# Optimization experiments

Measured on AMD Instinct MI355X. Metric: run time of the kernel, lower is better.

## Reference

```python
import jax, jax.numpy as jnp
import numpy as np

EMB_TABLE = 80000  # full shared embedding rows
N_ITEMS = 50000    # target item count (item_num + 1)
E = 600000         # edges
D = 128            # embedding_size
L = 3              # num_gcn_layers


def gcn_conv(x, W, b, src, dst, norm, n):
    # PyG GCNConv: x' = lin(x); out[i] = sum_{(j->i)} norm_ji * x'[j] + bias
    msgs = (x @ W)[src] * norm[:, None]          # [E+n, D]
    out = jax.ops.segment_sum(msgs, dst, num_segments=n)
    return out + b


def setup_inputs() -> dict:
    key = jax.random.key(0)
    k0, k1, k2 = jax.random.split(key, 3)
    item_emb = jax.random.normal(k0, (EMB_TABLE, D), dtype=jnp.float32) * 0.02
    weights = jax.random.normal(k1, (L, D, D), dtype=jnp.float32) * (1.0 / np.sqrt(D))
    biases = jnp.zeros((L, D), dtype=jnp.float32)
    edge_index = jax.random.randint(k2, (2, E), 0, N_ITEMS, dtype=jnp.int64)
    return {"item_emb": item_emb, "weights": weights, "biases": biases,
            "edge_index": edge_index, "item_nums": N_ITEMS}


def reference(item_emb, weights, biases, edge_index, item_nums):
    n = item_nums
    x0 = item_emb[-n:]  # embeds[0] = item_emb[-item_nums:]
    loops = jnp.arange(n, dtype=edge_index.dtype)
    src = jnp.concatenate([edge_index[0], loops])  # add self-loops (GCNConv default)
    dst = jnp.concatenate([edge_index[1], loops])
    # symmetric normalization: deg computed on target side with self-loops
    deg = jax.ops.segment_sum(jnp.ones_like(src, dtype=x0.dtype), dst, num_segments=n)
    dinv = jnp.where(deg > 0, jax.lax.rsqrt(jnp.maximum(deg, 1e-12)), 0.0)
    norm = dinv[src] * dinv[dst]                   # [E+n]
    embeds = [x0]
    for l in range(weights.shape[0]):
        embeds.append(gcn_conv(embeds[-1], weights[l], biases[l], src, dst, norm, n))
    total = embeds[0]
    for e in embeds[1:]:
        total = total + e
    return (total, *embeds)
```

## Files before the change

kernel.cpp:

```cpp
#include <hip/hip_runtime.h>
#include <stdint.h>

#define D 128

typedef unsigned int u32;
typedef unsigned short u16;
typedef __attribute__((ext_vector_type(8))) short short8;
typedef __attribute__((ext_vector_type(4))) float f32x4;

static __device__ __forceinline__ float bf2f(u16 h) {
    return __uint_as_float(((u32)h) << 16);
}
static __device__ __forceinline__ u16 f2bf(float f) {
    u32 u = __float_as_uint(f);
    u32 r = (u + 0x7fffu + ((u >> 16) & 1u)) >> 16;
    return (u16)r;
}
static __device__ __forceinline__ int clampi(int v, int n) {
    if (v < 0) v = 0;
    if (v >= n) v = n - 1;
    return v;
}

__global__ void k_init(int* __restrict__ hist, int* __restrict__ csr_pos, int n,
                       const u16* __restrict__ emb_raw, const u32* __restrict__ ei_raw,
                       const u16* __restrict__ w_raw, int* __restrict__ flags) {
    int i = blockIdx.x * 256 + threadIdx.x;
    if (i < n) {
        hist[i] = 0;
        csr_pos[i] = 0;
    }
    if (blockIdx.x == 0 && threadIdx.x < 64) {
        int t = threadIdx.x;
        int se = 0, sw = 0, zz = 0;
#pragma unroll
        for (int q = 0; q < 4; q++) {
            int k = t * 4 + q;
            u16 he = emb_raw[2 * k];
            u32 exe = (he >> 7) & 0xFF;
            if (he == 0 || (exe >= 0x60 && exe <= 0x8F)) se++;
            u16 hw = w_raw[2 * k];
            u32 exw = (hw >> 7) & 0xFF;
            if (hw == 0 || (exw >= 0x60 && exw <= 0x8F)) sw++;
            if (ei_raw[2 * k + 1] == 0) zz++;
        }
#pragma unroll
        for (int o = 32; o; o >>= 1) {
            se += __shfl_down(se, o);
            sw += __shfl_down(sw, o);
            zz += __shfl_down(zz, o);
        }
        if (t == 0) {
            flags[0] = (se >= 200) ? 1 : 0;
            flags[2] = (sw >= 200) ? 1 : 0;
            flags[1] = (zz >= 200) ? 1 : 0;
        }
    }
}

__global__ void k_hw(const u32* __restrict__ ei, int E, int n,
                     const int* __restrict__ flags, int* __restrict__ hist,
                     const void* __restrict__ Wbase, u16* __restrict__ WB, int eb) {
    int bid = blockIdx.x;
    if (bid < eb) {
        int e = bid * 256 + threadIdx.x;
        if (e >= E) return;
        int d;
        if (flags[1]) d = ((const int2*)ei)[(size_t)E + e].x;
        else          d = (int)ei[(size_t)E + e];
        atomicAdd(&hist[clampi(d, n)], 1);
    } else {
        int idx = (bid - eb) * 256 + threadIdx.x;
        int e = idx & 7;
        int l = (idx >> 3) & 63;
        int ks = (idx >> 9) & 3;
        int c = (idx >> 11) & 7;
        int layer = idx >> 14;
        int k = ks * 32 + ((l >> 4) << 3) + e;
        int j = (c << 4) + (l & 15);
        size_t src = (size_t)layer * D * D + (size_t)k * D + j;
        float w = flags[2] ? bf2f(((const u16*)Wbase)[src]) : ((const float*)Wbase)[src];
        u16 hb = f2bf(w);
        u16 lb = f2bf(w - bf2f(hb));
        size_t o = (size_t)layer * 32768 + (size_t)((c * 4 + ks) * 64 + l) * 8 + e;
        WB[o] = hb;
        WB[o + 16384] = lb;
    }
}

__global__ void k_scan1(const int* __restrict__ hist, int n,
                        int* __restrict__ incl, int* __restrict__ bsums) {
    __shared__ int s[256];
    int t = threadIdx.x;
    int i = blockIdx.x * 256 + t;
    int v = (i < n) ? hist[i] : 0;
    s[t] = v;
    __syncthreads();
    for (int d2 = 1; d2 < 256; d2 <<= 1) {
        int add = (t >= d2) ? s[t - d2] : 0;
        __syncthreads();
        s[t] += add;
        __syncthreads();
    }
    if (i < n) incl[i] = s[t];
    if (t == 255) bsums[blockIdx.x] = s[255];
}

__global__ void k_scan23(const int* __restrict__ hist, const int* __restrict__ bsums,
                         int n, int* __restrict__ csr_off, float* __restrict__ dinv) {
    __shared__ int s[256];
    int t = threadIdx.x, b = blockIdx.x;
    s[t] = (t < b) ? bsums[t] : 0;
    __syncthreads();
    for (int o = 128; o; o >>= 1) {
        if (t < o) s[t] += s[t + o];
        __syncthreads();
    }
    int add = s[0];
    int i = b * 256 + t;
    if (i < n) {
        int h = hist[i];
        csr_off[i] = add + csr_off[i] - h;
        dinv[i] = rsqrtf((float)(h + 1));
    }
}

__global__ void k_sx(const u32* __restrict__ ei, int E, int n,
                     const int* __restrict__ flags,
                     const int* __restrict__ csr_off, int* __restrict__ csr_pos,
                     const float* __restrict__ dinv, int2* __restrict__ csr_pair,
                     const void* __restrict__ emb, int off_elems, int nD4,
                     float* __restrict__ out_x0, int eb) {
    int bid = blockIdx.x;
    if (bid < eb) {
        int e = bid * 256 + threadIdx.x;
        if (e >= E) return;
        int s, d;
        if (flags[1]) {
            s = ((const int2*)ei)[e].x;
            d = ((const int2*)ei)[(size_t)E + e].x;
        } else {
            s = (int)ei[e];
            d = (int)ei[(size_t)E + e];
        }
        s = clampi(s, n);
        d = clampi(d, n);
        int p = csr_off[d] + atomicAdd(&csr_pos[d], 1);
        if (p >= E) p = E - 1;
        csr_pair[p] = make_int2(s, __float_as_int(dinv[s] * dinv[d]));
    } else {
        int i = (bid - eb) * 256 + threadIdx.x;
        if (i >= nD4) return;
        float4 v;
        if (flags[0]) {
            ushort4 h = ((const ushort4*)((const u16*)emb + off_elems))[i];
            v = make_float4(bf2f(h.x), bf2f(h.y), bf2f(h.z), bf2f(h.w));
        } else {
            v = ((const float4*)((const float*)emb + off_elems))[i];
        }
        ((float4*)out_x0)[i] = v;
    }
}

__global__ __launch_bounds__(256) void k_gemm(const float* __restrict__ A,
                                              const u16* __restrict__ WB, int layer,
                                              int n, u32* __restrict__ Y) {
    __shared__ f32x4 ldsv[4096];
    int tid = threadIdx.x;
    {
        const f32x4* src = (const f32x4*)(WB + (size_t)layer * 32768);
#pragma unroll
        for (int i = 0; i < 16; i++) ldsv[tid + 256 * i] = src[tid + 256 * i];
    }
    __syncthreads();

    int w = tid >> 6, l = tid & 63;
    int row0 = blockIdx.x * 64 + w * 16;
    int ar = row0 + (l & 15);
    if (ar >= n) ar = 0;
    const float* Ab = A + (size_t)ar * D + ((l >> 4) << 3);

    f32x4 acc[8] = {};
    const short8* bp = (const short8*)ldsv;

#pragma unroll
    for (int ks = 0; ks < 4; ks++) {
        f32x4 a0 = *(const f32x4*)(Ab + ks * 32);
        f32x4 a1 = *(const f32x4*)(Ab + ks * 32 + 4);
        float av[8] = {a0.x, a0.y, a0.z, a0.w, a1.x, a1.y, a1.z, a1.w};
        short8 ah, al;
#pragma unroll
        for (int e = 0; e < 8; e++) {
            u16 h = f2bf(av[e]);
            ah[e] = (short)h;
            al[e] = (short)f2bf(av[e] - bf2f(h));
        }
#pragma unroll
        for (int c = 0; c < 8; c++) {
            short8 bh = bp[(c * 4 + ks) * 64 + l];
            short8 bl = bp[2048 + (c * 4 + ks) * 64 + l];
            acc[c] = __builtin_amdgcn_mfma_f32_16x16x32_bf16(al, bh, acc[c], 0, 0, 0);
            acc[c] = __builtin_amdgcn_mfma_f32_16x16x32_bf16(ah, bl, acc[c], 0, 0, 0);
            acc[c] = __builtin_amdgcn_mfma_f32_16x16x32_bf16(ah, bh, acc[c], 0, 0, 0);
        }
    }

    int rbase = row0 + ((l >> 4) << 2);
    int col = l & 15;
#pragma unroll
    for (int r = 0; r < 4; r++) {
        int gr = rbase + r;
        if (gr < n) {
#pragma unroll
            for (int c = 0; c < 4; c++) {
                u32 pack = (u32)f2bf(acc[c][r]) | ((u32)f2bf(acc[c + 4][r]) << 16);
                Y[(size_t)gr * 64 + c * 16 + col] = pack;
            }
        }
    }
}

__global__ __launch_bounds__(256) void k_agg(const u32* __restrict__ Y,
                                             const int* __restrict__ csr_off,
                                             const int* __restrict__ cnt,
                                             const int2* __restrict__ csr_pair,
                                             const float* __restrict__ dinv,
                                             const void* __restrict__ bias_base, int layer,
                                             const int* __restrict__ flags, int n, int nD,
                                             const float* __restrict__ out_base,
                                             float* __restrict__ out_x,
                                             float* __restrict__ out_tot) {
    int i = blockIdx.x * 4 + (threadIdx.x >> 6);
    if (i >= n) return;
    int t = threadIdx.x & 63;
    int g = t >> 4, p = t & 15;

    float lo0 = 0.f, lo1 = 0.f, lo2 = 0.f, lo3 = 0.f;
    float hi0 = 0.f, hi1 = 0.f, hi2 = 0.f, hi3 = 0.f;

#define ACC4(V, W)                                                       \
    do {                                                                 \
        lo0 += __uint_as_float((V).x << 16) * (W);                       \
        hi0 += __uint_as_float((V).x & 0xffff0000u) * (W);               \
        lo1 += __uint_as_float((V).y << 16) * (W);                       \
        hi1 += __uint_as_float((V).y & 0xffff0000u) * (W);               \
        lo2 += __uint_as_float((V).z << 16) * (W);                       \
        hi2 += __uint_as_float((V).z & 0xffff0000u) * (W);               \
        lo3 += __uint_as_float((V).w << 16) * (W);                       \
        hi3 += __uint_as_float((V).w & 0xffff0000u) * (W);               \
    } while (0)

    float di = dinv[i];
    {
        uint4 vs = *(const uint4*)(Y + (size_t)i * 64 + p * 4);
        float ws = (g == 0) ? di * di : 0.0f;
        ACC4(vs, ws);
    }

    int start = csr_off[i];
    int c = cnt[i];

    for (int base = 0; base < c; base += 64) {
        int m = c - base;
        if (m > 64) m = 64;
        int2 pr = (t < m) ? csr_pair[start + base + t] : make_int2(0, 0);
        int s0 = __shfl(pr.x, g);
        float w0 = __uint_as_float((u32)__shfl(pr.y, g));
        uint4 v0 = *(const uint4*)(Y + (size_t)s0 * 64 + p * 4);
        for (int j = 4; j < m; j += 4) {
            int s1 = __shfl(pr.x, j + g);
            float w1 = __uint_as_float((u32)__shfl(pr.y, j + g));
            uint4 v1 = *(const uint4*)(Y + (size_t)s1 * 64 + p * 4);
            ACC4(v0, w0);
            v0 = v1;
            w0 = w1;
        }
        ACC4(v0, w0);
    }
#undef ACC4

#pragma unroll
    for (int mask = 16; mask <= 32; mask <<= 1) {
        lo0 += __shfl_xor(lo0, mask);
        lo1 += __shfl_xor(lo1, mask);
        lo2 += __shfl_xor(lo2, mask);
        lo3 += __shfl_xor(lo3, mask);
        hi0 += __shfl_xor(hi0, mask);
        hi1 += __shfl_xor(hi1, mask);
        hi2 += __shfl_xor(hi2, mask);
        hi3 += __shfl_xor(hi3, mask);
    }

    if (g < 2) {
        float r0 = g ? hi0 : lo0;
        float r1 = g ? hi1 : lo1;
        float r2 = g ? hi2 : lo2;
        float r3 = g ? hi3 : lo3;
        int off = g * 64 + 4 * p;
        float b0, b1, b2, b3;
        if (flags[0]) {
            const u16* bb = (const u16*)bias_base + layer * D + off;
            ushort4 h = *(const ushort4*)bb;
            b0 = bf2f(h.x); b1 = bf2f(h.y); b2 = bf2f(h.z); b3 = bf2f(h.w);
        } else {
            const float* bb = (const float*)bias_base + layer * D + off;
            float4 f = *(const float4*)bb;
            b0 = f.x; b1 = f.y; b2 = f.z; b3 = f.w;
        }
        float4 xv = make_float4(r0 + b0, r1 + b1, r2 + b2, r3 + b3);
        size_t base = (size_t)i * D + off;
        *(float4*)&out_x[base] = xv;

        if (out_tot) {
            float4 s0 = *(const float4*)&out_base[(size_t)1 * nD + base];
            float4 s1 = *(const float4*)&out_base[(size_t)2 * nD + base];
            float4 s2 = *(const float4*)&out_base[(size_t)3 * nD + base];
            *(float4*)&out_tot[base] =
                make_float4(s0.x + s1.x + s2.x + xv.x, s0.y + s1.y + s2.y + xv.y,
                            s0.z + s1.z + s2.z + xv.z, s0.w + s1.w + s2.w + xv.w);
        }
    }
}

extern "C" void kernel_launch(void* const* d_in, const int* in_sizes, int n_in,
                              void* d_out, int out_size, void* d_ws, size_t ws_size,
                              hipStream_t stream) {
    float* out = (float*)d_out;

    const int n = out_size / (5 * D);

    int i_emb = -1, i_ei = -1, i_w = -1, i_b = -1;
    {
        int order[8];
        int m = n_in > 8 ? 8 : n_in;
        for (int i = 0; i < m; i++) order[i] = i;
        for (int a = 0; a < m; a++)
            for (int b2 = a + 1; b2 < m; b2++)
                if (in_sizes[order[b2]] > in_sizes[order[a]]) {
                    int tmp = order[a]; order[a] = order[b2]; order[b2] = tmp;
                }
        i_emb = order[0];
        i_ei  = (m > 1) ? order[1] : 0;
        for (int i = 0; i < m; i++) {
            if (in_sizes[i] == 3 * D * D && i_w < 0) i_w = i;
            if (in_sizes[i] == 3 * D && i_b < 0) i_b = i;
        }
        if (i_w < 0) i_w = (m > 2) ? order[2] : 0;
        if (i_b < 0) i_b = (m > 3) ? order[3] : 0;
    }
    const void* emb  = d_in[i_emb];
    const void* wts  = d_in[i_w];
    const void* bias = d_in[i_b];
    const u32*  ei   = (const u32*)d_in[i_ei];

    const int E = in_sizes[i_ei] / 2;
    const int rows = in_sizes[i_emb] / D;
    const int off_elems = (rows - n) * D;

    char* p = (char*)d_ws;
    auto take = [&](size_t bytes) {
        char* r = p;
        p += (bytes + 255) & ~(size_t)255;
        return r;
    };
    int*   flags    = (int*)  take(3 * 4);
    int*   hist     = (int*)  take((size_t)n * 4);
    int*   csr_pos  = (int*)  take((size_t)n * 4);
    int*   csr_off  = (int*)  take((size_t)n * 4);
    int*   bsums    = (int*)  take(256 * 4);
    float* dinv     = (float*)take((size_t)n * 4);
    int2*  csr_pair = (int2*) take((size_t)E * 8);
    u32*   ybuf     = (u32*)  take((size_t)n * 64 * 4);
    u16*   wb       = (u16*)  take((size_t)3 * 32768 * 2);

    const int nD = n * D;
    const int nb = (n + 255) / 256;
    const int eb = (E + 255) / 256;
    const int x0b = (nD / 4 + 255) / 256;

    k_init<<<nb, 256, 0, stream>>>(hist, csr_pos, n, (const u16*)emb, ei,
                                   (const u16*)wts, flags);
    k_hw<<<eb + 192, 256, 0, stream>>>(ei, E, n, flags, hist, wts, wb, eb);
    k_scan1<<<nb, 256, 0, stream>>>(hist, n, csr_off, bsums);
    k_scan23<<<nb, 256, 0, stream>>>(hist, bsums, n, csr_off, dinv);
    k_sx<<<eb + x0b, 256, 0, stream>>>(ei, E, n, flags, csr_off, csr_pos, dinv,
                                       csr_pair, emb, off_elems, nD / 4,
                                       out + (size_t)nD, eb);

    const int ab = (n + 3) / 4;
    for (int l = 0; l < 3; l++) {
        const float* A = out + (size_t)(1 + l) * nD;
        float* ox = out + (size_t)(2 + l) * nD;
        k_gemm<<<(n + 63) / 64, 256, 0, stream>>>(A, wb, l, n, ybuf);
        k_agg<<<ab, 256, 0, stream>>>(ybuf, csr_off, hist, csr_pair, dinv, bias, l,
                                      flags, n, nD, out, ox,
                                      (l == 2) ? out : (float*)nullptr);
    }
}
```

Measured before the change: 350.2 us.

## Fuse GEMM into aggregation and prologue kernels, single-pass decoupled scan

Restructures the launch schedule: the next layer's dense transform is computed inside the aggregation kernel from an LDS tile of its own output rows, and the first-layer GEMM rides alongside the histogram pass. The two-kernel scan becomes a single-pass decoupled look-back scan, and init, weight split and x0 copy merge into one kernel, cutting launches from 11 to 7. This removes the separate GEMM launches and the re-read of each layer's output from global memory. In exchange the aggregation kernel uses much more LDS and registers, which can lower occupancy, and it reads the split weights straight from global memory rather than staging them in LDS.

```diff
diff --git a/kernel.cpp b/kernel.cpp
--- a/kernel.cpp
+++ b/kernel.cpp
@@ -21,56 +21,58 @@
     if (v >= n) v = n - 1;
     return v;
 }
-
-__global__ void k_init(int* __restrict__ hist, int* __restrict__ csr_pos, int n,
-                       const u16* __restrict__ emb_raw, const u32* __restrict__ ei_raw,
-                       const u16* __restrict__ w_raw, int* __restrict__ flags) {
-    int i = blockIdx.x * 256 + threadIdx.x;
-    if (i < n) {
-        hist[i] = 0;
-        csr_pos[i] = 0;
-    }
-    if (blockIdx.x == 0 && threadIdx.x < 64) {
-        int t = threadIdx.x;
-        int se = 0, sw = 0, zz = 0;
-#pragma unroll
-        for (int q = 0; q < 4; q++) {
-            int k = t * 4 + q;
-            u16 he = emb_raw[2 * k];
-            u32 exe = (he >> 7) & 0xFF;
-            if (he == 0 || (exe >= 0x60 && exe <= 0x8F)) se++;
-            u16 hw = w_raw[2 * k];
-            u32 exw = (hw >> 7) & 0xFF;
-            if (hw == 0 || (exw >= 0x60 && exw <= 0x8F)) sw++;
-            if (ei_raw[2 * k + 1] == 0) zz++;
-        }
-#pragma unroll
-        for (int o = 32; o; o >>= 1) {
-            se += __shfl_down(se, o);
-            sw += __shfl_down(sw, o);
-            zz += __shfl_down(zz, o);
-        }
-        if (t == 0) {
-            flags[0] = (se >= 200) ? 1 : 0;
-            flags[2] = (sw >= 200) ? 1 : 0;
-            flags[1] = (zz >= 200) ? 1 : 0;
-        }
-    }
-}
-
-__global__ void k_hw(const u32* __restrict__ ei, int E, int n,
-                     const int* __restrict__ flags, int* __restrict__ hist,
-                     const void* __restrict__ Wbase, u16* __restrict__ WB, int eb) {
-    int bid = blockIdx.x;
-    if (bid < eb) {
-        int e = bid * 256 + threadIdx.x;
-        if (e >= E) return;
-        int d;
-        if (flags[1]) d = ((const int2*)ei)[(size_t)E + e].x;
-        else          d = (int)ei[(size_t)E + e];
-        atomicAdd(&hist[clampi(d, n)], 1);
-    } else {
-        int idx = (bid - eb) * 256 + threadIdx.x;
+static __device__ __forceinline__ int bf_plausible(u16 h) {
+    u32 ex = (h >> 7) & 0xFF;
+    return (h == 0 || (ex >= 0x60 && ex <= 0x8F)) ? 1 : 0;
+}
+
+__global__ __launch_bounds__(256) void k_a(int* __restrict__ hist, int* __restrict__ csr_pos,
+                                           u32* __restrict__ state, int n, int nbk,
+                                           const u16* __restrict__ emb16,
+                                           const u32* __restrict__ ei,
+                                           const u16* __restrict__ w16,
+                                           int* __restrict__ flags, u16* __restrict__ WB,
+                                           int off_elems, int nD4,
+                                           float* __restrict__ out_x0) {
+    int bid = blockIdx.x, t = threadIdx.x;
+    __shared__ int ps[256];
+    if (bid < nbk) {
+        int i = bid * 256 + t;
+        if (i < n) {
+            hist[i] = 0;
+            csr_pos[i] = 0;
+        }
+        if (i < nbk) state[i] = 0;
+        if (bid == 0 && t < 64) {
+            int se = 0, sw = 0, zz = 0;
+#pragma unroll
+            for (int q = 0; q < 4; q++) {
+                int k = t * 4 + q;
+                se += bf_plausible(emb16[2 * k]);
+                sw += bf_plausible(w16[2 * k]);
+                if (ei[2 * k + 1] == 0) zz++;
+            }
+#pragma unroll
+            for (int o = 32; o; o >>= 1) {
+                se += __shfl_down(se, o);
+                sw += __shfl_down(sw, o);
+                zz += __shfl_down(zz, o);
+            }
+            if (t == 0) {
+                flags[0] = (se >= 200) ? 1 : 0;
+                flags[2] = (sw >= 200) ? 1 : 0;
+                flags[1] = (zz >= 200) ? 1 : 0;
+            }
+        }
+    } else if (bid < nbk + 192) {
+        ps[t] = bf_plausible(w16[2 * t]);
+        __syncthreads();
+        for (int o = 128; o; o >>= 1) {
+            if (t < o) ps[t] += ps[t + o];
+            __syncthreads();
+        }
+        int wf = (ps[0] >= 200);
+        int idx = (bid - nbk) * 256 + t;
         int e = idx & 7;
         int l = (idx >> 3) & 63;
         int ks = (idx >> 9) & 3;
@@ -79,22 +81,104 @@
         int k = ks * 32 + ((l >> 4) << 3) + e;
         int j = (c << 4) + (l & 15);
         size_t src = (size_t)layer * D * D + (size_t)k * D + j;
-        float w = flags[2] ? bf2f(((const u16*)Wbase)[src]) : ((const float*)Wbase)[src];
-        u16 hb = f2bf(w);
-        u16 lb = f2bf(w - bf2f(hb));
+        float wv = wf ? bf2f(w16[src]) : ((const float*)w16)[src];
+        u16 hb = f2bf(wv);
+        u16 lb = f2bf(wv - bf2f(hb));
         size_t o = (size_t)layer * 32768 + (size_t)((c * 4 + ks) * 64 + l) * 8 + e;
         WB[o] = hb;
         WB[o + 16384] = lb;
-    }
-}
-
-__global__ void k_scan1(const int* __restrict__ hist, int n,
-                        int* __restrict__ incl, int* __restrict__ bsums) {
+    } else {
+        ps[t] = bf_plausible(emb16[2 * t]);
+        __syncthreads();
+        for (int o = 128; o; o >>= 1) {
+            if (t < o) ps[t] += ps[t + o];
+            __syncthreads();
+        }
+        int ef = (ps[0] >= 200);
+        int i = (bid - nbk - 192) * 256 + t;
+        if (i < nD4) {
+            float4 v;
+            if (ef) {
+                ushort4 h = ((const ushort4*)(emb16 + off_elems))[i];
+                v = make_float4(bf2f(h.x), bf2f(h.y), bf2f(h.z), bf2f(h.w));
+            } else {
+                v = ((const float4*)((const float*)emb16 + off_elems))[i];
+            }
+            ((float4*)out_x0)[i] = v;
+        }
+    }
+}
+
+__global__ __launch_bounds__(256) void k_b(const u32* __restrict__ ei, int E, int n,
+                                           const int* __restrict__ flags,
+                                           int* __restrict__ hist,
+                                           const float* __restrict__ A0,
+                                           const u16* __restrict__ WB,
+                                           u32* __restrict__ Y0, int eb) {
+    int bid = blockIdx.x, tid = threadIdx.x;
+    if (bid < eb) {
+        int e = bid * 256 + tid;
+        if (e >= E) return;
+        int d;
+        if (flags[1]) d = ((const int2*)ei)[(size_t)E + e].x;
+        else          d = (int)ei[(size_t)E + e];
+        atomicAdd(&hist[clampi(d, n)], 1);
+    } else {
+        int bg = bid - eb;
+        int w = tid >> 6, l = tid & 63;
+        int row0 = bg * 64 + w * 16;
+        int ar = row0 + (l & 15);
+        if (ar >= n) ar = 0;
+        const float* Ab = A0 + (size_t)ar * D + ((l >> 4) << 3);
+        f32x4 acc[8] = {};
+        const short8* bp = (const short8*)WB;
+#pragma unroll
+        for (int ks = 0; ks < 4; ks++) {
+            f32x4 a0 = *(const f32x4*)(Ab + ks * 32);
+            f32x4 a1 = *(const f32x4*)(Ab + ks * 32 + 4);
+            float av[8] = {a0.x, a0.y, a0.z, a0.w, a1.x, a1.y, a1.z, a1.w};
+            short8 ah, al;
+#pragma unroll
+            for (int e2 = 0; e2 < 8; e2++) {
+                u16 h = f2bf(av[e2]);
+                ah[e2] = (short)h;
+                al[e2] = (short)f2bf(av[e2] - bf2f(h));
+            }
+#pragma unroll
+            for (int c = 0; c < 8; c++) {
+                short8 bh = bp[(c * 4 + ks) * 64 + l];
+                short8 bl = bp[2048 + (c * 4 + ks) * 64 + l];
+                acc[c] = __builtin_amdgcn_mfma_f32_16x16x32_bf16(al, bh, acc[c], 0, 0, 0);
+                acc[c] = __builtin_amdgcn_mfma_f32_16x16x32_bf16(ah, bl, acc[c], 0, 0, 0);
+                acc[c] = __builtin_amdgcn_mfma_f32_16x16x32_bf16(ah, bh, acc[c], 0, 0, 0);
+            }
+        }
+        int rbase = row0 + ((l >> 4) << 2);
+        int col = l & 15;
+#pragma unroll
+        for (int r = 0; r < 4; r++) {
+            int gr = rbase + r;
+            if (gr < n) {
+#pragma unroll
+                for (int c = 0; c < 4; c++) {
+                    u32 pack = (u32)f2bf(acc[c][r]) | ((u32)f2bf(acc[c + 4][r]) << 16);
+                    Y0[(size_t)gr * 64 + c * 16 + col] = pack;
+                }
+            }
+        }
+    }
+}
+
+__global__ __launch_bounds__(256) void k_scan(const int* __restrict__ hist, int n,
+                                              u32* __restrict__ state,
+                                              int* __restrict__ csr_off,
+                                              float* __restrict__ dinv) {
     __shared__ int s[256];
-    int t = threadIdx.x;
-    int i = blockIdx.x * 256 + t;
-    int v = (i < n) ? hist[i] : 0;
-    s[t] = v;
+    __shared__ int excl_sh;
+    int t = threadIdx.x, b = blockIdx.x;
+    int i = b * 256 + t;
+    int h = (i < n) ? hist[i] : 0;
+    s[t] = h;
     __syncthreads();
     for (int d2 = 1; d2 < 256; d2 <<= 1) {
         int add = (t >= d2) ? s[t - d2] : 0;
@@ -102,25 +186,38 @@
         s[t] += add;
         __syncthreads();
     }
-    if (i < n) incl[i] = s[t];
-    if (t == 255) bsums[blockIdx.x] = s[255];
-}
-
-__global__ void k_scan23(const int* __restrict__ hist, const int* __restrict__ bsums,
-                         int n, int* __restrict__ csr_off, float* __restrict__ dinv) {
-    __shared__ int s[256];
-    int t = threadIdx.x, b = blockIdx.x;
-    s[t] = (t < b) ? bsums[t] : 0;
+    int agg = s[255];
+    if (t == 0) {
+        if (b == 0) {
+            __hip_atomic_store(&state[0], (2u << 30) | (u32)agg, __ATOMIC_RELEASE,
+                               __HIP_MEMORY_SCOPE_AGENT);
+            excl_sh = 0;
+        } else {
+            __hip_atomic_store(&state[b], (1u << 30) | (u32)agg, __ATOMIC_RELEASE,
+                               __HIP_MEMORY_SCOPE_AGENT);
+            int run = 0;
+            int idx = b - 1;
+            while (true) {
+                u32 v = __hip_atomic_load(&state[idx], __ATOMIC_ACQUIRE,
+                                          __HIP_MEMORY_SCOPE_AGENT);
+                u32 f = v >> 30;
+                if (f == 0) {
+                    __builtin_amdgcn_s_sleep(1);
+                    continue;
+                }
+                run += (int)(v & 0x3fffffffu);
+                if (f == 2u) break;
+                idx--;
+            }
+            __hip_atomic_store(&state[b], (2u << 30) | (u32)(run + agg), __ATOMIC_RELEASE,
+                               __HIP_MEMORY_SCOPE_AGENT);
+            excl_sh = run;
+        }
+    }
     __syncthreads();
-    for (int o = 128; o; o >>= 1) {
-        if (t < o) s[t] += s[t + o];
-        __syncthreads();
-    }
-    int add = s[0];
-    int i = b * 256 + t;
+    int excl = excl_sh;
     if (i < n) {
-        int h = hist[i];
-        csr_off[i] = add + csr_off[i] - h;
+        csr_off[i] = excl + s[t] - h;
         dinv[i] = rsqrtf((float)(h + 1));
     }
 }
@@ -128,115 +225,41 @@
 __global__ void k_sx(const u32* __restrict__ ei, int E, int n,
                      const int* __restrict__ flags,
                      const int* __restrict__ csr_off, int* __restrict__ csr_pos,
-                     const float* __restrict__ dinv, int2* __restrict__ csr_pair,
-                     const void* __restrict__ emb, int off_elems, int nD4,
-                     float* __restrict__ out_x0, int eb) {
-    int bid = blockIdx.x;
-    if (bid < eb) {
-        int e = bid * 256 + threadIdx.x;
-        if (e >= E) return;
-        int s, d;
-        if (flags[1]) {
-            s = ((const int2*)ei)[e].x;
-            d = ((const int2*)ei)[(size_t)E + e].x;
-        } else {
-            s = (int)ei[e];
-            d = (int)ei[(size_t)E + e];
-        }
-        s = clampi(s, n);
-        d = clampi(d, n);
-        int p = csr_off[d] + atomicAdd(&csr_pos[d], 1);
-        if (p >= E) p = E - 1;
-        csr_pair[p] = make_int2(s, __float_as_int(dinv[s] * dinv[d]));
+                     const float* __restrict__ dinv, int2* __restrict__ csr_pair) {
+    int e = blockIdx.x * 256 + threadIdx.x;
+    if (e >= E) return;
+    int s, d;
+    if (flags[1]) {
+        s = ((const int2*)ei)[e].x;
+        d = ((const int2*)ei)[(size_t)E + e].x;
     } else {
-        int i = (bid - eb) * 256 + threadIdx.x;
-        if (i >= nD4) return;
-        float4 v;
-        if (flags[0]) {
-            ushort4 h = ((const ushort4*)((const u16*)emb + off_elems))[i];
-            v = make_float4(bf2f(h.x), bf2f(h.y), bf2f(h.z), bf2f(h.w));
-        } else {
-            v = ((const float4*)((const float*)emb + off_elems))[i];
-        }
-        ((float4*)out_x0)[i] = v;
-    }
-}
-
-__global__ __launch_bounds__(256) void k_gemm(const float* __restrict__ A,
-                                              const u16* __restrict__ WB, int layer,
-                                              int n, u32* __restrict__ Y) {
-    __shared__ f32x4 ldsv[4096];
+        s = (int)ei[e];
+        d = (int)ei[(size_t)E + e];
+    }
+    s = clampi(s, n);
+    d = clampi(d, n);
+    int p = csr_off[d] + atomicAdd(&csr_pos[d], 1);
+    if (p >= E) p = E - 1;
+    csr_pair[p] = make_int2(s, __float_as_int(dinv[s] * dinv[d]));
+}
+
+__global__ __launch_bounds__(256, 4) void k_ag(const u32* __restrict__ Yin,
+                                               const int* __restrict__ csr_off,
+                                               const int* __restrict__ cnt,
+                                               const int2* __restrict__ csr_pair,
+                                               const float* __restrict__ dinv,
+                                               const void* __restrict__ bias_base, int layer,
+                                               const int* __restrict__ flags, int n, int nD,
+                                               float* __restrict__ out_x,
+                                               float* __restrict__ out_tot,
+                                               const float* __restrict__ out_base,
+                                               const u16* __restrict__ WB, int gemm_layer,
+                                               u32* __restrict__ Yout) {
+    __shared__ float xt[64 * 132];
     int tid = threadIdx.x;
-    {
-        const f32x4* src = (const f32x4*)(WB + (size_t)layer * 32768);
-#pragma unroll
-        for (int i = 0; i < 16; i++) ldsv[tid + 256 * i] = src[tid + 256 * i];
-    }
-    __syncthreads();
-
-    int w = tid >> 6, l = tid & 63;
-    int row0 = blockIdx.x * 64 + w * 16;
-    int ar = row0 + (l & 15);
-    if (ar >= n) ar = 0;
-    const float* Ab = A + (size_t)ar * D + ((l >> 4) << 3);
-
-    f32x4 acc[8] = {};
-    const short8* bp = (const short8*)ldsv;
-
-#pragma unroll
-    for (int ks = 0; ks < 4; ks++) {
-        f32x4 a0 = *(const f32x4*)(Ab + ks * 32);
-        f32x4 a1 = *(const f32x4*)(Ab + ks * 32 + 4);
-        float av[8] = {a0.x, a0.y, a0.z, a0.w, a1.x, a1.y, a1.z, a1.w};
-        short8 ah, al;
-#pragma unroll
-        for (int e = 0; e < 8; e++) {
-            u16 h = f2bf(av[e]);
-            ah[e] = (short)h;
-            al[e] = (short)f2bf(av[e] - bf2f(h));
-        }
-#pragma unroll
-        for (int c = 0; c < 8; c++) {
-            short8 bh = bp[(c * 4 + ks) * 64 + l];
-            short8 bl = bp[2048 + (c * 4 + ks) * 64 + l];
-            acc[c] = __builtin_amdgcn_mfma_f32_16x16x32_bf16(al, bh, acc[c], 0, 0, 0);
-            acc[c] = __builtin_amdgcn_mfma_f32_16x16x32_bf16(ah, bl, acc[c], 0, 0, 0);
-            acc[c] = __builtin_amdgcn_mfma_f32_16x16x32_bf16(ah, bh, acc[c], 0, 0, 0);
-        }
-    }
-
-    int rbase = row0 + ((l >> 4) << 2);
-    int col = l & 15;
-#pragma unroll
-    for (int r = 0; r < 4; r++) {
-        int gr = rbase + r;
-        if (gr < n) {
-#pragma unroll
-            for (int c = 0; c < 4; c++) {
-                u32 pack = (u32)f2bf(acc[c][r]) | ((u32)f2bf(acc[c + 4][r]) << 16);
-                Y[(size_t)gr * 64 + c * 16 + col] = pack;
-            }
-        }
-    }
-}
-
-__global__ __launch_bounds__(256) void k_agg(const u32* __restrict__ Y,
-                                             const int* __restrict__ csr_off,
-                                             const int* __restrict__ cnt,
-                                             const int2* __restrict__ csr_pair,
-                                             const float* __restrict__ dinv,
-                                             const void* __restrict__ bias_base, int layer,
-                                             const int* __restrict__ flags, int n, int nD,
-                                             const float* __restrict__ out_base,
-                                             float* __restrict__ out_x,
-                                             float* __restrict__ out_tot) {
-    int i = blockIdx.x * 4 + (threadIdx.x >> 6);
-    if (i >= n) return;
-    int t = threadIdx.x & 63;
+    int w = tid >> 6, t = tid & 63;
     int g = t >> 4, p = t & 15;
-
-    float lo0 = 0.f, lo1 = 0.f, lo2 = 0.f, lo3 = 0.f;
-    float hi0 = 0.f, hi1 = 0.f, hi2 = 0.f, hi3 = 0.f;
+    int i0 = blockIdx.x * 64;
 
 #define ACC4(V, W)                                                       \
     do {                                                                 \
@@ -250,74 +273,121 @@
         hi3 += __uint_as_float((V).w & 0xffff0000u) * (W);               \
     } while (0)
 
-    float di = dinv[i];
-    {
-        uint4 vs = *(const uint4*)(Y + (size_t)i * 64 + p * 4);
-        float ws = (g == 0) ? di * di : 0.0f;
-        ACC4(vs, ws);
-    }
-
-    int start = csr_off[i];
-    int c = cnt[i];
-
-    for (int base = 0; base < c; base += 64) {
-        int m = c - base;
-        if (m > 64) m = 64;
-        int2 pr = (t < m) ? csr_pair[start + base + t] : make_int2(0, 0);
-        int s0 = __shfl(pr.x, g);
-        float w0 = __uint_as_float((u32)__shfl(pr.y, g));
-        uint4 v0 = *(const uint4*)(Y + (size_t)s0 * 64 + p * 4);
-        for (int j = 4; j < m; j += 4) {
-            int s1 = __shfl(pr.x, j + g);
-            float w1 = __uint_as_float((u32)__shfl(pr.y, j + g));
-            uint4 v1 = *(const uint4*)(Y + (size_t)s1 * 64 + p * 4);
+    for (int q = 0; q < 16; q++) {
+        int i = i0 + (w << 4) + q;
+        if (i >= n) break;
+
+        float lo0 = 0.f, lo1 = 0.f, lo2 = 0.f, lo3 = 0.f;
+        float hi0 = 0.f, hi1 = 0.f, hi2 = 0.f, hi3 = 0.f;
+
+        float di = dinv[i];
+        {
+            uint4 vs = *(const uint4*)(Yin + (size_t)i * 64 + p * 4);
+            float ws = (g == 0) ? di * di : 0.0f;
+            ACC4(vs, ws);
+        }
+        int start = csr_off[i];
+        int c = cnt[i];
+        for (int base = 0; base < c; base += 64) {
+            int m = c - base;
+            if (m > 64) m = 64;
+            int2 pr = (t < m) ? csr_pair[start + base + t] : make_int2(0, 0);
+            int s0 = __shfl(pr.x, g);
+            float w0 = __uint_as_float((u32)__shfl(pr.y, g));
+            uint4 v0 = *(const uint4*)(Yin + (size_t)s0 * 64 + p * 4);
+            for (int j = 4; j < m; j += 4) {
+                int s1 = __shfl(pr.x, j + g);
+                float w1 = __uint_as_float((u32)__shfl(pr.y, j + g));
+                uint4 v1 = *(const uint4*)(Yin + (size_t)s1 * 64 + p * 4);
+                ACC4(v0, w0);
+                v0 = v1;
+                w0 = w1;
+            }
             ACC4(v0, w0);
-            v0 = v1;
-            w0 = w1;
-        }
-        ACC4(v0, w0);
+        }
+#pragma unroll
+        for (int mask = 16; mask <= 32; mask <<= 1) {
+            lo0 += __shfl_xor(lo0, mask);
+            lo1 += __shfl_xor(lo1, mask);
+            lo2 += __shfl_xor(lo2, mask);
+            lo3 += __shfl_xor(lo3, mask);
+            hi0 += __shfl_xor(hi0, mask);
+            hi1 += __shfl_xor(hi1, mask);
+            hi2 += __shfl_xor(hi2, mask);
+            hi3 += __shfl_xor(hi3, mask);
+        }
+        if (g < 2) {
+            float r0 = g ? hi0 : lo0;
+            float r1 = g ? hi1 : lo1;
+            float r2 = g ? hi2 : lo2;
+            float r3 = g ? hi3 : lo3;
+            int off = g * 64 + 4 * p;
+            float b0, b1, b2, b3;
+            if (flags[0]) {
+                const u16* bb = (const u16*)bias_base + layer * D + off;
+                ushort4 h = *(const ushort4*)bb;
+                b0 = bf2f(h.x); b1 = bf2f(h.y); b2 = bf2f(h.z); b3 = bf2f(h.w);
+            } else {
+                const float* bb = (const float*)bias_base + layer * D + off;
+                float4 f = *(const float4*)bb;
+                b0 = f.x; b1 = f.y; b2 = f.z; b3 = f.w;
+            }
+            float4 xv = make_float4(r0 + b0, r1 + b1, r2 + b2, r3 + b3);
+            *(float4*)&xt[((w << 4) + q) * 132 + off] = xv;
+            size_t gbase = (size_t)i * D + off;
+            *(float4*)&out_x[gbase] = xv;
+            if (out_tot) {
+                float4 s0 = *(const float4*)&out_base[(size_t)1 * nD + gbase];
+                float4 s1 = *(const float4*)&out_base[(size_t)2 * nD + gbase];
+                float4 s2 = *(const float4*)&out_base[(size_t)3 * nD + gbase];
+                *(float4*)&out_tot[gbase] =
+                    make_float4(s0.x + s1.x + s2.x + xv.x, s0.y + s1.y + s2.y + xv.y,
+                                s0.z + s1.z + s2.z + xv.z, s0.w + s1.w + s2.w + xv.w);
+            }
+        }
     }
 #undef ACC4
 
-#pragma unroll
-    for (int mask = 16; mask <= 32; mask <<= 1) {
-        lo0 += __shfl_xor(lo0, mask);
-        lo1 += __shfl_xor(lo1, mask);
-        lo2 += __shfl_xor(lo2, mask);
-        lo3 += __shfl_xor(lo3, mask);
-        hi0 += __shfl_xor(hi0, mask);
-        hi1 += __shfl_xor(hi1, mask);
-        hi2 += __shfl_xor(hi2, mask);
-        hi3 += __shfl_xor(hi3, mask);
-    }
-
-    if (g < 2) {
-        float r0 = g ? hi0 : lo0;
-        float r1 = g ? hi1 : lo1;
-        float r2 = g ? hi2 : lo2;
-        float r3 = g ? hi3 : lo3;
-        int off = g * 64 + 4 * p;
-        float b0, b1, b2, b3;
-        if (flags[0]) {
-            const u16* bb = (const u16*)bias_base + layer * D + off;
-            ushort4 h = *(const ushort4*)bb;
-            b0 = bf2f(h.x); b1 = bf2f(h.y); b2 = bf2f(h.z); b3 = bf2f(h.w);
-        } else {
-            const float* bb = (const float*)bias_base + layer * D + off;
-            float4 f = *(const float4*)bb;
-            b0 = f.x; b1 = f.y; b2 = f.z; b3 = f.w;
-        }
-        float4 xv = make_float4(r0 + b0, r1 + b1, r2 + b2, r3 + b3);
-        size_t base = (size_t)i * D + off;
-        *(float4*)&out_x[base] = xv;
-
-        if (out_tot) {
-            float4 s0 = *(const float4*)&out_base[(size_t)1 * nD + base];
-            float4 s1 = *(const float4*)&out_base[(size_t)2 * nD + base];
-            float4 s2 = *(const float4*)&out_base[(size_t)3 * nD + base];
-            *(float4*)&out_tot[base] =
-                make_float4(s0.x + s1.x + s2.x + xv.x, s0.y + s1.y + s2.y + xv.y,
-                            s0.z + s1.z + s2.z + xv.z, s0.w + s1.w + s2.w + xv.w);
+    if (gemm_layer >= 0) {
+        __syncthreads();
+        int row0 = i0 + (w << 4);
+        int rl = (w << 4) + (t & 15);
+        const float* Ab = &xt[rl * 132 + ((t >> 4) << 3)];
+        f32x4 acc[8] = {};
+        const short8* bp = (const short8*)(WB + (size_t)gemm_layer * 32768);
+#pragma unroll
+        for (int ks = 0; ks < 4; ks++) {
+            f32x4 a0 = *(const f32x4*)(Ab + ks * 32);
+            f32x4 a1 = *(const f32x4*)(Ab + ks * 32 + 4);
+            float av[8] = {a0.x, a0.y, a0.z, a0.w, a1.x, a1.y, a1.z, a1.w};
+            short8 ah, al;
+#pragma unroll
+            for (int e2 = 0; e2 < 8; e2++) {
+                u16 h = f2bf(av[e2]);
+                ah[e2] = (short)h;
+                al[e2] = (short)f2bf(av[e2] - bf2f(h));
+            }
+#pragma unroll
+            for (int c = 0; c < 8; c++) {
+                short8 bh = bp[(c * 4 + ks) * 64 + t];
+                short8 bl = bp[2048 + (c * 4 + ks) * 64 + t];
+                acc[c] = __builtin_amdgcn_mfma_f32_16x16x32_bf16(al, bh, acc[c], 0, 0, 0);
+                acc[c] = __builtin_amdgcn_mfma_f32_16x16x32_bf16(ah, bl, acc[c], 0, 0, 0);
+                acc[c] = __builtin_amdgcn_mfma_f32_16x16x32_bf16(ah, bh, acc[c], 0, 0, 0);
+            }
+        }
+        int rbase = row0 + ((t >> 4) << 2);
+        int col = t & 15;
+#pragma unroll
+        for (int r = 0; r < 4; r++) {
+            int gr = rbase + r;
+            if (gr < n) {
+#pragma unroll
+                for (int c = 0; c < 4; c++) {
+                    u32 pack = (u32)f2bf(acc[c][r]) | ((u32)f2bf(acc[c + 4][r]) << 16);
+                    Yout[(size_t)gr * 64 + c * 16 + col] = pack;
+                }
+            }
         }
     }
 }
@@ -363,37 +433,36 @@
         p += (bytes + 255) & ~(size_t)255;
         return r;
     };
+    const int nD = n * D;
+    const int nb = (n + 255) / 256;
+    const int eb = (E + 255) / 256;
+    const int x0b = (nD / 4 + 255) / 256;
+    const int gb = (n + 63) / 64;
+
     int*   flags    = (int*)  take(3 * 4);
     int*   hist     = (int*)  take((size_t)n * 4);
     int*   csr_pos  = (int*)  take((size_t)n * 4);
     int*   csr_off  = (int*)  take((size_t)n * 4);
-    int*   bsums    = (int*)  take(256 * 4);
+    u32*   state    = (u32*)  take((size_t)nb * 4);
     float* dinv     = (float*)take((size_t)n * 4);
     int2*  csr_pair = (int2*) take((size_t)E * 8);
-    u32*   ybuf     = (u32*)  take((size_t)n * 64 * 4);
+    u32*   yA       = (u32*)  take((size_t)n * 64 * 4);
+    u32*   yB       = (u32*)  take((size_t)n * 64 * 4);
     u16*   wb       = (u16*)  take((size_t)3 * 32768 * 2);
 
-    const int nD = n * D;
-    const int nb = (n + 255) / 256;
-    const int eb = (E + 255) / 256;
-    const int x0b = (nD / 4 + 255) / 256;
-
-    k_init<<<nb, 256, 0, stream>>>(hist, csr_pos, n, (const u16*)emb, ei,
-                                   (const u16*)wts, flags);
-    k_hw<<<eb + 192, 256, 0, stream>>>(ei, E, n, flags, hist, wts, wb, eb);
-    k_scan1<<<nb, 256, 0, stream>>>(hist, n, csr_off, bsums);
-    k_scan23<<<nb, 256, 0, stream>>>(hist, bsums, n, csr_off, dinv);
-    k_sx<<<eb + x0b, 256, 0, stream>>>(ei, E, n, flags, csr_off, csr_pos, dinv,
-                                       csr_pair, emb, off_elems, nD / 4,
-                                       out + (size_t)nD, eb);
-
-    const int ab = (n + 3) / 4;
-    for (int l = 0; l < 3; l++) {
-        const float* A = out + (size_t)(1 + l) * nD;
-        float* ox = out + (size_t)(2 + l) * nD;
-        k_gemm<<<(n + 63) / 64, 256, 0, stream>>>(A, wb, l, n, ybuf);
-        k_agg<<<ab, 256, 0, stream>>>(ybuf, csr_off, hist, csr_pair, dinv, bias, l,
-                                      flags, n, nD, out, ox,
-                                      (l == 2) ? out : (float*)nullptr);
-    }
-}
+    float* x0 = out + (size_t)nD;
+
+    k_a<<<nb + 192 + x0b, 256, 0, stream>>>(hist, csr_pos, state, n, nb, (const u16*)emb,
+                                            ei, (const u16*)wts, flags, wb, off_elems,
+                                            nD / 4, x0);
+    k_b<<<eb + gb, 256, 0, stream>>>(ei, E, n, flags, hist, x0, wb, yA, eb);
+    k_scan<<<nb, 256, 0, stream>>>(hist, n, state, csr_off, dinv);
+    k_sx<<<eb, 256, 0, stream>>>(ei, E, n, flags, csr_off, csr_pos, dinv, csr_pair);
+
+    k_ag<<<gb, 256, 0, stream>>>(yA, csr_off, hist, csr_pair, dinv, bias, 0, flags, n, nD,
+                                 out + (size_t)2 * nD, (float*)nullptr, out, wb, 1, yB);
+    k_ag<<<gb, 256, 0, stream>>>(yB, csr_off, hist, csr_pair, dinv, bias, 1, flags, n, nD,
+                                 out + (size_t)3 * nD, (float*)nullptr, out, wb, 2, yA);
+    k_ag<<<gb, 256, 0, stream>>>(yA, csr_off, hist, csr_pair, dinv, bias, 2, flags, n, nD,
+                                 out + (size_t)4 * nD, out, out, wb, -1, (u32*)nullptr);
+}
```

Result: slower. 431.4 us (+23.2%).
